# Kernel optimization log

Hardware: AMD Instinct MI355X
Metric: run time of the kernel (lower is better)

The kernel has to match this reference:

```python
import jax, jax.numpy as jnp
import numpy as np

# OmniNet(deepqmc) reconstruction: ElectronicSchNet v1 (2 interactions, kernel_dim=8,
# embedding_dim=16, dist_feat_dim=4) + Linear(16,1,bias=False) orbital + sum over electrons.
# SchNet v1: shared w and g per interaction, spin-dependent h (same/anti), nuclear
# messages via learned nuclear embeddings Y. Subnets: w = 2-layer log-DNN 4->6->8 with SSP,
# h = Linear(16,8), g = Linear(8,16). SSP(x) = softplus(x) - log(2).

N_UP, N_DOWN = 16, 16
N_ELEC = N_UP + N_DOWN
N_ATOMS = 8
DIST_FEAT, KERNEL, EMBED = 4, 8, 16
N_INTER = 2
BATCH = 4096


def ssp(x):
    return jax.nn.softplus(x) - jnp.log(2.0).astype(x.dtype)


def setup_inputs() -> dict:
    key = jax.random.key(0)
    ks = jax.random.split(key, 16)
    s = 0.5  # init scale
    return {
        'dists_nuc': jax.random.uniform(ks[0], (BATCH, N_ELEC, N_ATOMS, DIST_FEAT), jnp.float32),
        'dists_elec': jax.random.uniform(ks[1], (BATCH, N_ELEC, N_ELEC, DIST_FEAT), jnp.float32),
        'X': jax.random.normal(ks[2], (1, EMBED), jnp.float32) * s,          # electron embedding (n_up==n_down)
        'Y': jax.random.normal(ks[3], (N_ATOMS, KERNEL), jnp.float32) * s,   # nuclear embeddings
        'w1': jax.random.normal(ks[4], (N_INTER, DIST_FEAT, 6), jnp.float32) * s,
        'wb1': jax.random.normal(ks[5], (N_INTER, 6), jnp.float32) * s,
        'w2': jax.random.normal(ks[6], (N_INTER, 6, KERNEL), jnp.float32) * s,
        'wb2': jax.random.normal(ks[7], (N_INTER, KERNEL), jnp.float32) * s,
        'hs_w': jax.random.normal(ks[8], (N_INTER, EMBED, KERNEL), jnp.float32) * s,
        'hs_b': jax.random.normal(ks[9], (N_INTER, KERNEL), jnp.float32) * s,
        'ha_w': jax.random.normal(ks[10], (N_INTER, EMBED, KERNEL), jnp.float32) * s,
        'ha_b': jax.random.normal(ks[11], (N_INTER, KERNEL), jnp.float32) * s,
        'g_w': jax.random.normal(ks[12], (N_INTER, KERNEL, EMBED), jnp.float32) * s,
        'g_b': jax.random.normal(ks[13], (N_INTER, EMBED), jnp.float32) * s,
        'orb_w': jax.random.normal(ks[14], (EMBED,), jnp.float32) * s,
    }


def reference(dists_nuc, dists_elec, X, Y, w1, wb1, w2, wb2, hs_w, hs_b, ha_w, ha_b, g_w, g_b, orb_w):
    B, n_elec = dists_elec.shape[:2]
    dt = dists_elec.dtype
    spins = jnp.concatenate([jnp.zeros(N_UP, jnp.int32), jnp.ones(N_DOWN, jnp.int32)])
    eye = jnp.eye(n_elec, dtype=bool)
    same = ((spins[:, None] == spins[None, :]) & ~eye).astype(dt)  # (i,j) same-spin, no self
    anti = (spins[:, None] != spins[None, :]).astype(dt)

    # initial embeddings: all electrons share X[0] since n_up == n_down
    x = jnp.broadcast_to(X[0], (B, n_elec, EMBED))

    for n in range(N_INTER):
        def w_net(e):  # (..., 4) -> (..., 8)
            return ssp(e @ w1[n] + wb1[n]) @ w2[n] + wb2[n]
        we = w_net(dists_elec)            # (B, i, j, K)
        wn = w_net(dists_nuc)             # (B, i, M, K)
        hs = x @ hs_w[n] + hs_b[n]        # (B, j, K) same-spin message features
        ha = x @ ha_w[n] + ha_b[n]        # (B, j, K) anti-spin
        z = (jnp.einsum('bijk,ij,bjk->bik', we, same, hs)
             + jnp.einsum('bijk,ij,bjk->bik', we, anti, ha)
             + jnp.einsum('bimk,mk->bik', wn, Y))
        x = x + (z @ g_w[n] + g_b[n])     # residual update

    # orbital projection (Linear(16,1,bias=False)), squeeze, sum over electrons
    return (x @ orb_w).sum(axis=-1)       # (B,)
```

## Files before the change

kernel.cpp:

```cpp
#include <hip/hip_runtime.h>

#define NE 32
#define NA 8
#define DF 4
#define KD 8
#define ED 16
#define BATCH 4096

#define WS_W1S0 0
#define WS_W1S1 24
#define WS_B1S0 48
#define WS_B1S1 54
#define WS_B2H0 60
#define WS_B2H1 68
#define WS_MS0  76
#define WS_MA0  84
#define WS_MS   92
#define WS_MA   156
#define WS_CS   220
#define WS_CA   228
#define WS_GO0  236
#define WS_GO1  244
#define WS_BASE 252

typedef float f32x2 __attribute__((ext_vector_type(2)));
__device__ __forceinline__ f32x2 splat2(float s) { f32x2 r; r.x = s; r.y = s; return r; }
__device__ __forceinline__ f32x2 fma2(f32x2 a, f32x2 b, f32x2 c) {
    return __builtin_elementwise_fma(a, b, c);
}

__global__ void omni_setup(const float* __restrict__ X,   const float* __restrict__ w1,
                           const float* __restrict__ wb1, const float* __restrict__ w2,
                           const float* __restrict__ wb2, const float* __restrict__ hs_w,
                           const float* __restrict__ hs_b,const float* __restrict__ ha_w,
                           const float* __restrict__ ha_b,const float* __restrict__ g_w,
                           const float* __restrict__ g_b, const float* __restrict__ orb_w,
                           float* __restrict__ ws)
{
    const int t = threadIdx.x;
    const float L   = 1.4426950408889634f;
    const float LN2 = 0.6931471805599453f;
    if (t < 48) {
        ws[t] = w1[t] * L;
    } else if (t < 60) {
        ws[t] = wb1[t - 48] * L;
    } else if (t < 76) {
        const int u = t - 60, n = u >> 3, k = u & 7;
        float sw = 0.f;
        for (int a = 0; a < 6; ++a) sw += w2[n * 48 + a * KD + k];
        ws[t] = wb2[n * KD + k] * L - sw;
    } else if (t < 92) {
        const int u = t - 76, tab = u >> 3, k = u & 7;
        const float* mw = tab ? ha_w : hs_w;
        const float* mb = tab ? ha_b : hs_b;
        float acc = mb[k];
        for (int c = 0; c < ED; ++c) acc += X[c] * mw[c * KD + k];
        ws[t] = acc;
    } else if (t < 220) {
        int u = t - 92; const int tab = u >> 6; u &= 63;
        const int kp = u >> 3, k = u & 7;
        const float* mw = (tab ? ha_w : hs_w) + ED * KD;
        float acc = 0.f;
        for (int c = 0; c < ED; ++c)
            acc += LN2 * g_w[kp * ED + c] * mw[c * KD + k];
        ws[t] = acc;
    } else if (t < 236) {
        const int u = t - 220, tab = u >> 3, k = u & 7;
        const float* mw = (tab ? ha_w : hs_w) + ED * KD;
        const float* mb = (tab ? ha_b : hs_b) + KD;
        float acc = mb[k];
        for (int c = 0; c < ED; ++c) acc += (X[c] + g_b[c]) * mw[c * KD + k];
        ws[t] = acc;
    } else if (t < 252) {
        const int u = t - 236, n = u >> 3, k = u & 7;
        float acc = 0.f;
        for (int c = 0; c < ED; ++c)
            acc += LN2 * g_w[n * KD * ED + k * ED + c] * orb_w[c];
        ws[t] = acc;
    } else if (t == 252) {
        float acc = 0.f;
        for (int c = 0; c < ED; ++c) acc += (X[c] + g_b[c] + g_b[ED + c]) * orb_w[c];
        ws[t] = acc;
    }
}

__device__ __forceinline__ void wnet_r2(const float4 e,
                                        const f32x2* __restrict__ vB1s2,
                                        const f32x2* __restrict__ sW12,
                                        f32x2* __restrict__ r2)
{
    #pragma unroll
    for (int a2 = 0; a2 < 3; ++a2) {
        f32x2 u = fma2(splat2(e.x), sW12[a2], vB1s2[a2]);
        u = fma2(splat2(e.y), sW12[3 + a2], u);
        u = fma2(splat2(e.z), sW12[6 + a2], u);
        u = fma2(splat2(e.w), sW12[9 + a2], u);
        f32x2 t;
        t.x = __builtin_amdgcn_exp2f(u.x);
        t.y = __builtin_amdgcn_exp2f(u.y);
        t = t + splat2(1.0f);
        r2[a2].x = __builtin_amdgcn_logf(t.x);
        r2[a2].y = __builtin_amdgcn_logf(t.y);
    }
}

__device__ __forceinline__ void proj2(const f32x2* __restrict__ r2,
                                      const f32x2* __restrict__ sW22,
                                      const f32x2* __restrict__ vB2h2,
                                      f32x2* __restrict__ racc2)
{
    #pragma unroll
    for (int k2 = 0; k2 < 4; ++k2) {
        f32x2 acc = vB2h2[k2];
        acc = fma2(splat2(r2[0].x), sW22[0 * 4 + k2], acc);
        acc = fma2(splat2(r2[0].y), sW22[1 * 4 + k2], acc);
        acc = fma2(splat2(r2[1].x), sW22[2 * 4 + k2], acc);
        acc = fma2(splat2(r2[1].y), sW22[3 * 4 + k2], acc);
        acc = fma2(splat2(r2[2].x), sW22[4 * 4 + k2], acc);
        acc = fma2(splat2(r2[2].y), sW22[5 * 4 + k2], acc);
        racc2[k2] = acc;
    }
}

__global__ __launch_bounds__(128)
__attribute__((amdgpu_waves_per_eu(3, 4)))
void omni_main(
    const float* __restrict__ dists_nuc,
    const float* __restrict__ dists_elec,
    const float* __restrict__ Y,
    const float* __restrict__ w2,
    const float* __restrict__ ws,
    float* __restrict__ out)
{
    const int tid  = threadIdx.x;
    const int h    = tid >> 6;
    const int lane = tid & 63;
    const int il   = lane & 15;
    const int jh   = lane >> 4;
    const int ig   = 16 * h + il;
    const int b    = blockIdx.x;
    const int sj   = jh >> 1;
    const bool same = (sj == h);
    const int t32  = same ? 0 : 32;

    __shared__ float msg[65][KD];
    __shared__ float part[2];
    if (tid < KD) msg[64][tid] = 0.0f;

    const f32x2* ws2  = (const f32x2*)ws;
    const f32x2* w2p0 = (const f32x2*)w2;
    const f32x2* w2p1 = (const f32x2*)(w2 + 48);
    const f32x2* Yp   = (const f32x2*)Y;

    const float* de = dists_elec + (((size_t)b * NE + ig) * NE + 8 * jh) * DF;
    const float* dn = dists_nuc  + (((size_t)b * NE + ig) * NA + 2 * jh) * DF;

    float4 er[8];
    float4 nr[2];
    #pragma unroll
    for (int s = 0; s < 8; ++s) er[s] = ((const float4*)de)[s];
    nr[0] = ((const float4*)dn)[0];
    nr[1] = ((const float4*)dn)[1];

    f32x2 racc1[40];

    float zr0[KD];
    {
        f32x2 vB1s0[3], vB1s1[3], vB2h0[4], vB2h1[4], msel2[4];
        #pragma unroll
        for (int a2 = 0; a2 < 3; ++a2) {
            vB1s0[a2] = ws2[WS_B1S0 / 2 + a2];
            vB1s1[a2] = ws2[WS_B1S1 / 2 + a2];
        }
        #pragma unroll
        for (int k2 = 0; k2 < 4; ++k2) {
            vB2h0[k2] = ws2[WS_B2H0 / 2 + k2];
            vB2h1[k2] = ws2[WS_B2H1 / 2 + k2];
            msel2[k2] = same ? ws2[WS_MS0 / 2 + k2] : ws2[WS_MA0 / 2 + k2];
        }

        const int scnt  = ig - 8 * jh;
        const float fcnt = (jh == (ig >> 3)) ? 7.0f : 8.0f;
        f32x2 S2[3] = {splat2(0.f), splat2(0.f), splat2(0.f)};
        #pragma unroll
        for (int s = 0; s < 8; ++s) {
            f32x2 r0[3], r1[3];
            wnet_r2(er[s], vB1s0, ws2 + WS_W1S0 / 2, r0);
            wnet_r2(er[s], vB1s1, ws2 + WS_W1S1 / 2, r1);
            const float mf = (s == scnt) ? 0.0f : 1.0f;
            #pragma unroll
            for (int a2 = 0; a2 < 3; ++a2) S2[a2] = fma2(r0[a2], splat2(mf), S2[a2]);
            proj2(r1, w2p1, vB2h1, &racc1[s * 4]);
        }
        f32x2 z2[4];
        #pragma unroll
        for (int k2 = 0; k2 < 4; ++k2) {
            f32x2 acc = splat2(fcnt) * vB2h0[k2];
            acc = fma2(splat2(S2[0].x), w2p0[0 * 4 + k2], acc);
            acc = fma2(splat2(S2[0].y), w2p0[1 * 4 + k2], acc);
            acc = fma2(splat2(S2[1].x), w2p0[2 * 4 + k2], acc);
            acc = fma2(splat2(S2[1].y), w2p0[3 * 4 + k2], acc);
            acc = fma2(splat2(S2[2].x), w2p0[4 * 4 + k2], acc);
            acc = fma2(splat2(S2[2].y), w2p0[5 * 4 + k2], acc);
            z2[k2] = acc * msel2[k2];
        }
        #pragma unroll
        for (int t = 0; t < 2; ++t) {
            f32x2 r0[3], r1[3], racc0[4];
            wnet_r2(nr[t], vB1s0, ws2 + WS_W1S0 / 2, r0);
            wnet_r2(nr[t], vB1s1, ws2 + WS_W1S1 / 2, r1);
            proj2(r0, w2p0, vB2h0, racc0);
            proj2(r1, w2p1, vB2h1, &racc1[(8 + t) * 4]);
            #pragma unroll
            for (int k2 = 0; k2 < 4; ++k2)
                z2[k2] = fma2(racc0[k2], Yp[(2 * jh + t) * 4 + k2], z2[k2]);
        }
        #pragma unroll
        for (int k2 = 0; k2 < 4; ++k2) {
            float za = z2[k2].x, zb = z2[k2].y;
            za += __shfl_xor(za, 16, 64); za += __shfl_xor(za, 32, 64);
            zb += __shfl_xor(zb, 16, 64); zb += __shfl_xor(zb, 32, 64);
            zr0[2 * k2] = za; zr0[2 * k2 + 1] = zb;
        }
    }

    {
        f32x2 ms2[4], ma2[4];
        #pragma unroll
        for (int k2 = 0; k2 < 4; ++k2) {
            ms2[k2] = ws2[WS_CS / 2 + k2];
            ma2[k2] = ws2[WS_CA / 2 + k2];
        }
        #pragma unroll
        for (int kp = 0; kp < KD; ++kp) {
            const f32x2 zk = splat2(zr0[kp]);
            #pragma unroll
            for (int k2 = 0; k2 < 4; ++k2) {
                ms2[k2] = fma2(zk, ws2[WS_MS / 2 + kp * 4 + k2], ms2[k2]);
                ma2[k2] = fma2(zk, ws2[WS_MA / 2 + kp * 4 + k2], ma2[k2]);
            }
        }
        if (jh == 0) {
            #pragma unroll
            for (int k2 = 0; k2 < 4; ++k2) *(f32x2*)&msg[ig][2 * k2] = ms2[k2];
        } else if (jh == 2) {
            #pragma unroll
            for (int k2 = 0; k2 < 4; ++k2) *(f32x2*)&msg[32 + ig][2 * k2] = ma2[k2];
        }
    }

    float dot = ws[WS_BASE];
    #pragma unroll
    for (int k = 0; k < KD; ++k) dot = fmaf(zr0[k], ws[WS_GO0 + k], dot);

    __syncthreads();

    float zr1[KD];
    {
        f32x2 z2[4] = {splat2(0.f), splat2(0.f), splat2(0.f), splat2(0.f)};
        #pragma unroll
        for (int s = 0; s < 8; ++s) {
            const int j = 8 * jh + s;
            const int row = (j == ig) ? 64 : (t32 + j);
            const f32x2* mrow = (const f32x2*)&msg[row][0];
            #pragma unroll
            for (int k2 = 0; k2 < 4; ++k2)
                z2[k2] = fma2(racc1[s * 4 + k2], mrow[k2], z2[k2]);
        }
        #pragma unroll
        for (int t = 0; t < 2; ++t) {
            #pragma unroll
            for (int k2 = 0; k2 < 4; ++k2)
                z2[k2] = fma2(racc1[(8 + t) * 4 + k2], Yp[(2 * jh + t) * 4 + k2], z2[k2]);
        }
        #pragma unroll
        for (int k2 = 0; k2 < 4; ++k2) {
            float za = z2[k2].x, zb = z2[k2].y;
            za += __shfl_xor(za, 16, 64); za += __shfl_xor(za, 32, 64);
            zb += __shfl_xor(zb, 16, 64); zb += __shfl_xor(zb, 32, 64);
            zr1[2 * k2] = za; zr1[2 * k2 + 1] = zb;
        }
    }

    #pragma unroll
    for (int k = 0; k < KD; ++k) dot = fmaf(zr1[k], ws[WS_GO1 + k], dot);
    dot *= 0.25f;
    #pragma unroll
    for (int off = 1; off < 64; off <<= 1) dot += __shfl_xor(dot, off, 64);
    if (lane == 0) part[h] = dot;
    __syncthreads();
    if (tid == 0) out[b] = part[0] + part[1];
}

extern "C" void kernel_launch(void* const* d_in, const int* in_sizes, int n_in,
                              void* d_out, int out_size, void* d_ws, size_t ws_size,
                              hipStream_t stream) {
    const float* dists_nuc  = (const float*)d_in[0];
    const float* dists_elec = (const float*)d_in[1];
    const float* X     = (const float*)d_in[2];
    const float* Y     = (const float*)d_in[3];
    const float* w1    = (const float*)d_in[4];
    const float* wb1   = (const float*)d_in[5];
    const float* w2    = (const float*)d_in[6];
    const float* wb2   = (const float*)d_in[7];
    const float* hs_w  = (const float*)d_in[8];
    const float* hs_b  = (const float*)d_in[9];
    const float* ha_w  = (const float*)d_in[10];
    const float* ha_b  = (const float*)d_in[11];
    const float* g_w   = (const float*)d_in[12];
    const float* g_b   = (const float*)d_in[13];
    const float* orb_w = (const float*)d_in[14];
    float* out = (float*)d_out;
    float* ws  = (float*)d_ws;

    omni_setup<<<1, 256, 0, stream>>>(X, w1, wb1, w2, wb2, hs_w, hs_b,
                                      ha_w, ha_b, g_w, g_b, orb_w, ws);
    omni_main<<<BATCH, 128, 0, stream>>>(dists_nuc, dists_elec, Y, w2, ws, out);
}
```

Measured before the change: 144.9 us.

## Stage electron distances in LDS and recompute layer-1 w-net to cut registers

Electron distance features are loaded once into shared memory instead of being held in registers. The second interaction's w-net outputs are recomputed inside the interaction-2 loop rather than kept in a 40-entry register array across the barrier. Loop unrolling is reduced and the waves-per-EU hint is removed. The aim is lower register pressure and higher occupancy for this memory-bound kernel, at the cost of extra LDS traffic (16 KB per block) and a second pass over the distance data.

```diff
diff --git a/kernel.cpp b/kernel.cpp
--- a/kernel.cpp
+++ b/kernel.cpp
@@ -123,7 +123,6 @@
 }
 
 __global__ __launch_bounds__(128)
-__attribute__((amdgpu_waves_per_eu(3, 4)))
 void omni_main(
     const float* __restrict__ dists_nuc,
     const float* __restrict__ dists_elec,
@@ -143,6 +142,7 @@
     const bool same = (sj == h);
     const int t32  = same ? 0 : 32;
 
+    __shared__ float4 ebuf[8 * 128];
     __shared__ float msg[65][KD];
     __shared__ float part[2];
     if (tid < KD) msg[64][tid] = 0.0f;
@@ -154,43 +154,44 @@
 
     const float* de = dists_elec + (((size_t)b * NE + ig) * NE + 8 * jh) * DF;
     const float* dn = dists_nuc  + (((size_t)b * NE + ig) * NA + 2 * jh) * DF;
-
-    float4 er[8];
-    float4 nr[2];
-    #pragma unroll
-    for (int s = 0; s < 8; ++s) er[s] = ((const float4*)de)[s];
-    nr[0] = ((const float4*)dn)[0];
-    nr[1] = ((const float4*)dn)[1];
-
-    f32x2 racc1[40];
+    const float4* de4 = (const float4*)de;
+
+    {
+        float4 t[8];
+        #pragma unroll
+        for (int s = 0; s < 8; ++s) t[s] = de4[s];
+        #pragma unroll
+        for (int s = 0; s < 8; ++s) ebuf[s * 128 + tid] = t[s];
+    }
+    const float4 nr0 = ((const float4*)dn)[0];
+    const float4 nr1 = ((const float4*)dn)[1];
+
+    f32x2 vB1s0[3], vB1s1[3], vB2h0[4], vB2h1[4], msel2[4];
+    #pragma unroll
+    for (int a2 = 0; a2 < 3; ++a2) {
+        vB1s0[a2] = ws2[WS_B1S0 / 2 + a2];
+        vB1s1[a2] = ws2[WS_B1S1 / 2 + a2];
+    }
+    #pragma unroll
+    for (int k2 = 0; k2 < 4; ++k2) {
+        vB2h0[k2] = ws2[WS_B2H0 / 2 + k2];
+        vB2h1[k2] = ws2[WS_B2H1 / 2 + k2];
+        msel2[k2] = same ? ws2[WS_MS0 / 2 + k2] : ws2[WS_MA0 / 2 + k2];
+    }
+    const int scnt   = ig - 8 * jh;
+    const float fcnt = (jh == (ig >> 3)) ? 7.0f : 8.0f;
 
     float zr0[KD];
     {
-        f32x2 vB1s0[3], vB1s1[3], vB2h0[4], vB2h1[4], msel2[4];
-        #pragma unroll
-        for (int a2 = 0; a2 < 3; ++a2) {
-            vB1s0[a2] = ws2[WS_B1S0 / 2 + a2];
-            vB1s1[a2] = ws2[WS_B1S1 / 2 + a2];
-        }
-        #pragma unroll
-        for (int k2 = 0; k2 < 4; ++k2) {
-            vB2h0[k2] = ws2[WS_B2H0 / 2 + k2];
-            vB2h1[k2] = ws2[WS_B2H1 / 2 + k2];
-            msel2[k2] = same ? ws2[WS_MS0 / 2 + k2] : ws2[WS_MA0 / 2 + k2];
-        }
-
-        const int scnt  = ig - 8 * jh;
-        const float fcnt = (jh == (ig >> 3)) ? 7.0f : 8.0f;
         f32x2 S2[3] = {splat2(0.f), splat2(0.f), splat2(0.f)};
-        #pragma unroll
+        #pragma unroll 2
         for (int s = 0; s < 8; ++s) {
-            f32x2 r0[3], r1[3];
-            wnet_r2(er[s], vB1s0, ws2 + WS_W1S0 / 2, r0);
-            wnet_r2(er[s], vB1s1, ws2 + WS_W1S1 / 2, r1);
+            const float4 e = ebuf[s * 128 + tid];
+            f32x2 r2[3];
+            wnet_r2(e, vB1s0, ws2 + WS_W1S0 / 2, r2);
             const float mf = (s == scnt) ? 0.0f : 1.0f;
             #pragma unroll
-            for (int a2 = 0; a2 < 3; ++a2) S2[a2] = fma2(r0[a2], splat2(mf), S2[a2]);
-            proj2(r1, w2p1, vB2h1, &racc1[s * 4]);
+            for (int a2 = 0; a2 < 3; ++a2) S2[a2] = fma2(r2[a2], splat2(mf), S2[a2]);
         }
         f32x2 z2[4];
         #pragma unroll
@@ -204,16 +205,15 @@
             acc = fma2(splat2(S2[2].y), w2p0[5 * 4 + k2], acc);
             z2[k2] = acc * msel2[k2];
         }
-        #pragma unroll
+        #pragma clang loop unroll(disable)
         for (int t = 0; t < 2; ++t) {
-            f32x2 r0[3], r1[3], racc0[4];
-            wnet_r2(nr[t], vB1s0, ws2 + WS_W1S0 / 2, r0);
-            wnet_r2(nr[t], vB1s1, ws2 + WS_W1S1 / 2, r1);
-            proj2(r0, w2p0, vB2h0, racc0);
-            proj2(r1, w2p1, vB2h1, &racc1[(8 + t) * 4]);
+            const float4 nt = t ? nr1 : nr0;
+            f32x2 r2[3], racc2[4];
+            wnet_r2(nt, vB1s0, ws2 + WS_W1S0 / 2, r2);
+            proj2(r2, w2p0, vB2h0, racc2);
             #pragma unroll
             for (int k2 = 0; k2 < 4; ++k2)
-                z2[k2] = fma2(racc0[k2], Yp[(2 * jh + t) * 4 + k2], z2[k2]);
+                z2[k2] = fma2(racc2[k2], Yp[(2 * jh + t) * 4 + k2], z2[k2]);
         }
         #pragma unroll
         for (int k2 = 0; k2 < 4; ++k2) {
@@ -258,20 +258,27 @@
     float zr1[KD];
     {
         f32x2 z2[4] = {splat2(0.f), splat2(0.f), splat2(0.f), splat2(0.f)};
-        #pragma unroll
+        #pragma unroll 2
         for (int s = 0; s < 8; ++s) {
+            const float4 e = ebuf[s * 128 + tid];
+            f32x2 r2[3], racc2[4];
+            wnet_r2(e, vB1s1, ws2 + WS_W1S1 / 2, r2);
+            proj2(r2, w2p1, vB2h1, racc2);
             const int j = 8 * jh + s;
             const int row = (j == ig) ? 64 : (t32 + j);
             const f32x2* mrow = (const f32x2*)&msg[row][0];
             #pragma unroll
+            for (int k2 = 0; k2 < 4; ++k2) z2[k2] = fma2(racc2[k2], mrow[k2], z2[k2]);
+        }
+        #pragma clang loop unroll(disable)
+        for (int t = 0; t < 2; ++t) {
+            const float4 nt = t ? nr1 : nr0;
+            f32x2 r2[3], racc2[4];
+            wnet_r2(nt, vB1s1, ws2 + WS_W1S1 / 2, r2);
+            proj2(r2, w2p1, vB2h1, racc2);
+            #pragma unroll
             for (int k2 = 0; k2 < 4; ++k2)
-                z2[k2] = fma2(racc1[s * 4 + k2], mrow[k2], z2[k2]);
-        }
-        #pragma unroll
-        for (int t = 0; t < 2; ++t) {
-            #pragma unroll
-            for (int k2 = 0; k2 < 4; ++k2)
-                z2[k2] = fma2(racc1[(8 + t) * 4 + k2], Yp[(2 * jh + t) * 4 + k2], z2[k2]);
+                z2[k2] = fma2(racc2[k2], Yp[(2 * jh + t) * 4 + k2], z2[k2]);
         }
         #pragma unroll
         for (int k2 = 0; k2 < 4; ++k2) {
```

Measured after the change: 145.2 us. No clear change (+0.2%).

## Process two batch items per block and recompute interaction-1 filters

Applied to the files above, without the earlier changes.

Each block now handles two batch elements, interleaving their computation so there is more independent work per thread and half as many blocks. The interaction-1 filter outputs are no longer held in a 40-entry register array. Instead they are recomputed in the second phase from one sample's distances staged in LDS and the other's kept in registers, with double message buffers. This trades extra ALU work and LDS traffic for lower register pressure, more ILP and fewer blocks, at the risk of occupancy changes from the larger shared memory and register footprint.

```diff
diff --git a/kernel.cpp b/kernel.cpp
--- a/kernel.cpp
+++ b/kernel.cpp
@@ -138,158 +138,227 @@
     const int il   = lane & 15;
     const int jh   = lane >> 4;
     const int ig   = 16 * h + il;
-    const int b    = blockIdx.x;
     const int sj   = jh >> 1;
     const bool same = (sj == h);
     const int t32  = same ? 0 : 32;
 
-    __shared__ float msg[65][KD];
-    __shared__ float part[2];
-    if (tid < KD) msg[64][tid] = 0.0f;
+    __shared__ float4 ebuf[8 * 128];
+    __shared__ float msgA[65][KD];
+    __shared__ float msgB[65][KD];
+    __shared__ float part[2][2];
+    if (tid < KD) { msgA[64][tid] = 0.0f; msgB[64][tid] = 0.0f; }
 
     const f32x2* ws2  = (const f32x2*)ws;
     const f32x2* w2p0 = (const f32x2*)w2;
     const f32x2* w2p1 = (const f32x2*)(w2 + 48);
     const f32x2* Yp   = (const f32x2*)Y;
 
-    const float* de = dists_elec + (((size_t)b * NE + ig) * NE + 8 * jh) * DF;
-    const float* dn = dists_nuc  + (((size_t)b * NE + ig) * NA + 2 * jh) * DF;
-
-    float4 er[8];
-    float4 nr[2];
-    #pragma unroll
-    for (int s = 0; s < 8; ++s) er[s] = ((const float4*)de)[s];
-    nr[0] = ((const float4*)dn)[0];
-    nr[1] = ((const float4*)dn)[1];
-
-    f32x2 racc1[40];
-
-    float zr0[KD];
+    const int b0 = 2 * blockIdx.x;
+    const float* deA = dists_elec + (((size_t)b0 * NE + ig) * NE + 8 * jh) * DF;
+    const float* dnA = dists_nuc  + (((size_t)b0 * NE + ig) * NA + 2 * jh) * DF;
+    const float* deB = deA + (size_t)NE * NE * DF;
+    const float* dnB = dnA + (size_t)NE * NA * DF;
+
+    float4 eA[8], eB[8];
+    #pragma unroll
+    for (int s = 0; s < 8; ++s) eA[s] = ((const float4*)deA)[s];
+    #pragma unroll
+    for (int s = 0; s < 8; ++s) eB[s] = ((const float4*)deB)[s];
+    const float4 nrA0 = ((const float4*)dnA)[0];
+    const float4 nrA1 = ((const float4*)dnA)[1];
+    const float4 nrB0 = ((const float4*)dnB)[0];
+    const float4 nrB1 = ((const float4*)dnB)[1];
+
+    float zr0A[KD], zr0B[KD];
     {
-        f32x2 vB1s0[3], vB1s1[3], vB2h0[4], vB2h1[4], msel2[4];
-        #pragma unroll
-        for (int a2 = 0; a2 < 3; ++a2) {
-            vB1s0[a2] = ws2[WS_B1S0 / 2 + a2];
-            vB1s1[a2] = ws2[WS_B1S1 / 2 + a2];
-        }
+        f32x2 vB1s0[3], vB2h0[4], msel2[4];
+        #pragma unroll
+        for (int a2 = 0; a2 < 3; ++a2) vB1s0[a2] = ws2[WS_B1S0 / 2 + a2];
         #pragma unroll
         for (int k2 = 0; k2 < 4; ++k2) {
             vB2h0[k2] = ws2[WS_B2H0 / 2 + k2];
-            vB2h1[k2] = ws2[WS_B2H1 / 2 + k2];
             msel2[k2] = same ? ws2[WS_MS0 / 2 + k2] : ws2[WS_MA0 / 2 + k2];
         }
-
-        const int scnt  = ig - 8 * jh;
+        const int scnt   = ig - 8 * jh;
         const float fcnt = (jh == (ig >> 3)) ? 7.0f : 8.0f;
-        f32x2 S2[3] = {splat2(0.f), splat2(0.f), splat2(0.f)};
+
+        f32x2 SA[3] = {splat2(0.f), splat2(0.f), splat2(0.f)};
+        f32x2 SB[3] = {splat2(0.f), splat2(0.f), splat2(0.f)};
         #pragma unroll
         for (int s = 0; s < 8; ++s) {
-            f32x2 r0[3], r1[3];
-            wnet_r2(er[s], vB1s0, ws2 + WS_W1S0 / 2, r0);
-            wnet_r2(er[s], vB1s1, ws2 + WS_W1S1 / 2, r1);
+            ebuf[s * 128 + tid] = eA[s];
+            f32x2 rA[3], rB[3];
+            wnet_r2(eA[s], vB1s0, ws2 + WS_W1S0 / 2, rA);
+            wnet_r2(eB[s], vB1s0, ws2 + WS_W1S0 / 2, rB);
             const float mf = (s == scnt) ? 0.0f : 1.0f;
             #pragma unroll
-            for (int a2 = 0; a2 < 3; ++a2) S2[a2] = fma2(r0[a2], splat2(mf), S2[a2]);
-            proj2(r1, w2p1, vB2h1, &racc1[s * 4]);
-        }
-        f32x2 z2[4];
-        #pragma unroll
-        for (int k2 = 0; k2 < 4; ++k2) {
-            f32x2 acc = splat2(fcnt) * vB2h0[k2];
-            acc = fma2(splat2(S2[0].x), w2p0[0 * 4 + k2], acc);
-            acc = fma2(splat2(S2[0].y), w2p0[1 * 4 + k2], acc);
-            acc = fma2(splat2(S2[1].x), w2p0[2 * 4 + k2], acc);
-            acc = fma2(splat2(S2[1].y), w2p0[3 * 4 + k2], acc);
-            acc = fma2(splat2(S2[2].x), w2p0[4 * 4 + k2], acc);
-            acc = fma2(splat2(S2[2].y), w2p0[5 * 4 + k2], acc);
-            z2[k2] = acc * msel2[k2];
+            for (int a2 = 0; a2 < 3; ++a2) {
+                SA[a2] = fma2(rA[a2], splat2(mf), SA[a2]);
+                SB[a2] = fma2(rB[a2], splat2(mf), SB[a2]);
+            }
+        }
+        f32x2 zA[4], zB[4];
+        #pragma unroll
+        for (int k2 = 0; k2 < 4; ++k2) {
+            f32x2 aA = splat2(fcnt) * vB2h0[k2];
+            f32x2 aB = aA;
+            aA = fma2(splat2(SA[0].x), w2p0[0 * 4 + k2], aA);
+            aB = fma2(splat2(SB[0].x), w2p0[0 * 4 + k2], aB);
+            aA = fma2(splat2(SA[0].y), w2p0[1 * 4 + k2], aA);
+            aB = fma2(splat2(SB[0].y), w2p0[1 * 4 + k2], aB);
+            aA = fma2(splat2(SA[1].x), w2p0[2 * 4 + k2], aA);
+            aB = fma2(splat2(SB[1].x), w2p0[2 * 4 + k2], aB);
+            aA = fma2(splat2(SA[1].y), w2p0[3 * 4 + k2], aA);
+            aB = fma2(splat2(SB[1].y), w2p0[3 * 4 + k2], aB);
+            aA = fma2(splat2(SA[2].x), w2p0[4 * 4 + k2], aA);
+            aB = fma2(splat2(SB[2].x), w2p0[4 * 4 + k2], aB);
+            aA = fma2(splat2(SA[2].y), w2p0[5 * 4 + k2], aA);
+            aB = fma2(splat2(SB[2].y), w2p0[5 * 4 + k2], aB);
+            zA[k2] = aA * msel2[k2];
+            zB[k2] = aB * msel2[k2];
         }
         #pragma unroll
         for (int t = 0; t < 2; ++t) {
-            f32x2 r0[3], r1[3], racc0[4];
-            wnet_r2(nr[t], vB1s0, ws2 + WS_W1S0 / 2, r0);
-            wnet_r2(nr[t], vB1s1, ws2 + WS_W1S1 / 2, r1);
-            proj2(r0, w2p0, vB2h0, racc0);
-            proj2(r1, w2p1, vB2h1, &racc1[(8 + t) * 4]);
-            #pragma unroll
-            for (int k2 = 0; k2 < 4; ++k2)
-                z2[k2] = fma2(racc0[k2], Yp[(2 * jh + t) * 4 + k2], z2[k2]);
-        }
-        #pragma unroll
-        for (int k2 = 0; k2 < 4; ++k2) {
-            float za = z2[k2].x, zb = z2[k2].y;
-            za += __shfl_xor(za, 16, 64); za += __shfl_xor(za, 32, 64);
-            zb += __shfl_xor(zb, 16, 64); zb += __shfl_xor(zb, 32, 64);
-            zr0[2 * k2] = za; zr0[2 * k2 + 1] = zb;
+            f32x2 rA[3], rB[3], pA[4], pB[4];
+            wnet_r2(t ? nrA1 : nrA0, vB1s0, ws2 + WS_W1S0 / 2, rA);
+            wnet_r2(t ? nrB1 : nrB0, vB1s0, ws2 + WS_W1S0 / 2, rB);
+            proj2(rA, w2p0, vB2h0, pA);
+            proj2(rB, w2p0, vB2h0, pB);
+            #pragma unroll
+            for (int k2 = 0; k2 < 4; ++k2) {
+                zA[k2] = fma2(pA[k2], Yp[(2 * jh + t) * 4 + k2], zA[k2]);
+                zB[k2] = fma2(pB[k2], Yp[(2 * jh + t) * 4 + k2], zB[k2]);
+            }
+        }
+        #pragma unroll
+        for (int k2 = 0; k2 < 4; ++k2) {
+            float zaA = zA[k2].x, zbA = zA[k2].y;
+            float zaB = zB[k2].x, zbB = zB[k2].y;
+            zaA += __shfl_xor(zaA, 16, 64); zaB += __shfl_xor(zaB, 16, 64);
+            zbA += __shfl_xor(zbA, 16, 64); zbB += __shfl_xor(zbB, 16, 64);
+            zaA += __shfl_xor(zaA, 32, 64); zaB += __shfl_xor(zaB, 32, 64);
+            zbA += __shfl_xor(zbA, 32, 64); zbB += __shfl_xor(zbB, 32, 64);
+            zr0A[2 * k2] = zaA; zr0A[2 * k2 + 1] = zbA;
+            zr0B[2 * k2] = zaB; zr0B[2 * k2 + 1] = zbB;
         }
     }
 
     {
-        f32x2 ms2[4], ma2[4];
-        #pragma unroll
-        for (int k2 = 0; k2 < 4; ++k2) {
-            ms2[k2] = ws2[WS_CS / 2 + k2];
-            ma2[k2] = ws2[WS_CA / 2 + k2];
+        f32x2 msA[4], maA[4], msB[4], maB[4];
+        #pragma unroll
+        for (int k2 = 0; k2 < 4; ++k2) {
+            msA[k2] = ws2[WS_CS / 2 + k2]; msB[k2] = msA[k2];
+            maA[k2] = ws2[WS_CA / 2 + k2]; maB[k2] = maA[k2];
         }
         #pragma unroll
         for (int kp = 0; kp < KD; ++kp) {
-            const f32x2 zk = splat2(zr0[kp]);
-            #pragma unroll
-            for (int k2 = 0; k2 < 4; ++k2) {
-                ms2[k2] = fma2(zk, ws2[WS_MS / 2 + kp * 4 + k2], ms2[k2]);
-                ma2[k2] = fma2(zk, ws2[WS_MA / 2 + kp * 4 + k2], ma2[k2]);
+            const f32x2 zkA = splat2(zr0A[kp]);
+            const f32x2 zkB = splat2(zr0B[kp]);
+            #pragma unroll
+            for (int k2 = 0; k2 < 4; ++k2) {
+                const f32x2 Mk = ws2[WS_MS / 2 + kp * 4 + k2];
+                const f32x2 Ak = ws2[WS_MA / 2 + kp * 4 + k2];
+                msA[k2] = fma2(zkA, Mk, msA[k2]);
+                msB[k2] = fma2(zkB, Mk, msB[k2]);
+                maA[k2] = fma2(zkA, Ak, maA[k2]);
+                maB[k2] = fma2(zkB, Ak, maB[k2]);
             }
         }
         if (jh == 0) {
             #pragma unroll
-            for (int k2 = 0; k2 < 4; ++k2) *(f32x2*)&msg[ig][2 * k2] = ms2[k2];
+            for (int k2 = 0; k2 < 4; ++k2) {
+                *(f32x2*)&msgA[ig][2 * k2] = msA[k2];
+                *(f32x2*)&msgB[ig][2 * k2] = msB[k2];
+            }
         } else if (jh == 2) {
             #pragma unroll
-            for (int k2 = 0; k2 < 4; ++k2) *(f32x2*)&msg[32 + ig][2 * k2] = ma2[k2];
-        }
-    }
-
-    float dot = ws[WS_BASE];
-    #pragma unroll
-    for (int k = 0; k < KD; ++k) dot = fmaf(zr0[k], ws[WS_GO0 + k], dot);
+            for (int k2 = 0; k2 < 4; ++k2) {
+                *(f32x2*)&msgA[32 + ig][2 * k2] = maA[k2];
+                *(f32x2*)&msgB[32 + ig][2 * k2] = maB[k2];
+            }
+        }
+    }
+
+    float dotA = ws[WS_BASE], dotB = ws[WS_BASE];
+    #pragma unroll
+    for (int k = 0; k < KD; ++k) {
+        dotA = fmaf(zr0A[k], ws[WS_GO0 + k], dotA);
+        dotB = fmaf(zr0B[k], ws[WS_GO0 + k], dotB);
+    }
 
     __syncthreads();
 
-    float zr1[KD];
+    float zr1A[KD], zr1B[KD];
     {
-        f32x2 z2[4] = {splat2(0.f), splat2(0.f), splat2(0.f), splat2(0.f)};
+        f32x2 vB1s1[3], vB2h1[4];
+        #pragma unroll
+        for (int a2 = 0; a2 < 3; ++a2) vB1s1[a2] = ws2[WS_B1S1 / 2 + a2];
+        #pragma unroll
+        for (int k2 = 0; k2 < 4; ++k2) vB2h1[k2] = ws2[WS_B2H1 / 2 + k2];
+
+        f32x2 zA[4] = {splat2(0.f), splat2(0.f), splat2(0.f), splat2(0.f)};
+        f32x2 zB[4] = {splat2(0.f), splat2(0.f), splat2(0.f), splat2(0.f)};
         #pragma unroll
         for (int s = 0; s < 8; ++s) {
+            const float4 a = ebuf[s * 128 + tid];
+            f32x2 rA[3], rB[3], pA[4], pB[4];
+            wnet_r2(a,     vB1s1, ws2 + WS_W1S1 / 2, rA);
+            wnet_r2(eB[s], vB1s1, ws2 + WS_W1S1 / 2, rB);
+            proj2(rA, w2p1, vB2h1, pA);
+            proj2(rB, w2p1, vB2h1, pB);
             const int j = 8 * jh + s;
             const int row = (j == ig) ? 64 : (t32 + j);
-            const f32x2* mrow = (const f32x2*)&msg[row][0];
-            #pragma unroll
-            for (int k2 = 0; k2 < 4; ++k2)
-                z2[k2] = fma2(racc1[s * 4 + k2], mrow[k2], z2[k2]);
+            const f32x2* mA = (const f32x2*)&msgA[row][0];
+            const f32x2* mB = (const f32x2*)&msgB[row][0];
+            #pragma unroll
+            for (int k2 = 0; k2 < 4; ++k2) {
+                zA[k2] = fma2(pA[k2], mA[k2], zA[k2]);
+                zB[k2] = fma2(pB[k2], mB[k2], zB[k2]);
+            }
         }
         #pragma unroll
         for (int t = 0; t < 2; ++t) {
-            #pragma unroll
-            for (int k2 = 0; k2 < 4; ++k2)
-                z2[k2] = fma2(racc1[(8 + t) * 4 + k2], Yp[(2 * jh + t) * 4 + k2], z2[k2]);
-        }
-        #pragma unroll
-        for (int k2 = 0; k2 < 4; ++k2) {
-            float za = z2[k2].x, zb = z2[k2].y;
-            za += __shfl_xor(za, 16, 64); za += __shfl_xor(za, 32, 64);
-            zb += __shfl_xor(zb, 16, 64); zb += __shfl_xor(zb, 32, 64);
-            zr1[2 * k2] = za; zr1[2 * k2 + 1] = zb;
-        }
-    }
-
-    #pragma unroll
-    for (int k = 0; k < KD; ++k) dot = fmaf(zr1[k], ws[WS_GO1 + k], dot);
-    dot *= 0.25f;
-    #pragma unroll
-    for (int off = 1; off < 64; off <<= 1) dot += __shfl_xor(dot, off, 64);
-    if (lane == 0) part[h] = dot;
+            f32x2 rA[3], rB[3], pA[4], pB[4];
+            wnet_r2(t ? nrA1 : nrA0, vB1s1, ws2 + WS_W1S1 / 2, rA);
+            wnet_r2(t ? nrB1 : nrB0, vB1s1, ws2 + WS_W1S1 / 2, rB);
+            proj2(rA, w2p1, vB2h1, pA);
+            proj2(rB, w2p1, vB2h1, pB);
+            #pragma unroll
+            for (int k2 = 0; k2 < 4; ++k2) {
+                zA[k2] = fma2(pA[k2], Yp[(2 * jh + t) * 4 + k2], zA[k2]);
+                zB[k2] = fma2(pB[k2], Yp[(2 * jh + t) * 4 + k2], zB[k2]);
+            }
+        }
+        #pragma unroll
+        for (int k2 = 0; k2 < 4; ++k2) {
+            float zaA = zA[k2].x, zbA = zA[k2].y;
+            float zaB = zB[k2].x, zbB = zB[k2].y;
+            zaA += __shfl_xor(zaA, 16, 64); zaB += __shfl_xor(zaB, 16, 64);
+            zbA += __shfl_xor(zbA, 16, 64); zbB += __shfl_xor(zbB, 16, 64);
+            zaA += __shfl_xor(zaA, 32, 64); zaB += __shfl_xor(zaB, 32, 64);
+            zbA += __shfl_xor(zbA, 32, 64); zbB += __shfl_xor(zbB, 32, 64);
+            zr1A[2 * k2] = zaA; zr1A[2 * k2 + 1] = zbA;
+            zr1B[2 * k2] = zaB; zr1B[2 * k2 + 1] = zbB;
+        }
+    }
+
+    #pragma unroll
+    for (int k = 0; k < KD; ++k) {
+        dotA = fmaf(zr1A[k], ws[WS_GO1 + k], dotA);
+        dotB = fmaf(zr1B[k], ws[WS_GO1 + k], dotB);
+    }
+    dotA *= 0.25f; dotB *= 0.25f;
+    #pragma unroll
+    for (int off = 1; off < 64; off <<= 1) {
+        dotA += __shfl_xor(dotA, off, 64);
+        dotB += __shfl_xor(dotB, off, 64);
+    }
+    if (lane == 0) { part[0][h] = dotA; part[1][h] = dotB; }
     __syncthreads();
-    if (tid == 0) out[b] = part[0] + part[1];
+    if (tid == 0) {
+        out[b0]     = part[0][0] + part[0][1];
+        out[b0 + 1] = part[1][0] + part[1][1];
+    }
 }
 
 extern "C" void kernel_launch(void* const* d_in, const int* in_sizes, int n_in,
@@ -315,5 +384,5 @@
 
     omni_setup<<<1, 256, 0, stream>>>(X, w1, wb1, w2, wb2, hs_w, hs_b,
                                       ha_w, ha_b, g_w, g_b, orb_w, ws);
-    omni_main<<<BATCH, 128, 0, stream>>>(dists_nuc, dists_elec, Y, w2, ws, out);
-}
+    omni_main<<<BATCH / 2, 128, 0, stream>>>(dists_nuc, dists_elec, Y, w2, ws, out);
+}
```

New measurement: 155.1 us. 7.1% more time.
